# Performance work log

Hardware: AMD Instinct MI355X
Metric: run time of the kernel (lower is better)

## Reference

```python
import jax, jax.numpy as jnp
import numpy as np

N_EMBED = 2048
N_HEAD = 16
HEAD_DIM = N_EMBED // N_HEAD  # 128


def setup_inputs() -> dict:
    key = jax.random.key(0)
    k1, k2, k3 = jax.random.split(key, 3)
    B, S = 2, 2048
    x = jax.random.normal(k1, (B, S, N_EMBED), dtype=jnp.float32)
    # torch Linear weight [out,in]; store transposed for x @ W
    scale_attn = 1.0 / np.sqrt(N_EMBED)
    w_attn = jax.random.normal(k2, (N_EMBED, (N_HEAD + 2) * HEAD_DIM), dtype=jnp.float32) * scale_attn
    w_out = jax.random.normal(k3, (N_EMBED, N_EMBED), dtype=jnp.float32) * scale_attn
    return {"x": x, "w_attn": w_attn, "w_out": w_out}


def reference(x, w_attn, w_out):
    B, S, E = x.shape
    H, D = N_HEAD, HEAD_DIM
    qkv = x @ w_attn                               # [B,S,(H+2)*D]
    q, k, v = jnp.split(qkv, [E, E + D], axis=2)   # [B,S,E], [B,S,D], [B,S,D]
    q = q.reshape(B, S, H, D).transpose(0, 2, 1, 3)  # [B,H,S,D]
    # single shared K/V head (MQA)
    scores = jnp.einsum("bhsd,btd->bhst", q, k) * (D ** -0.5)  # [B,H,S,S]
    p = jax.nn.softmax(scores, axis=-1)
    attn = jnp.einsum("bhst,btd->bhsd", p, v)      # [B,H,S,D]
    attn = attn.transpose(0, 2, 1, 3).reshape(B, S, E)
    return attn @ w_out
```

## Files before the change

### kernel.cpp

```cpp
#include <hip/hip_runtime.h>
#include <hip/hip_bf16.h>

typedef __attribute__((ext_vector_type(8))) short short8;
typedef __attribute__((ext_vector_type(4))) float f32x4;

#define GLOBAL_AS __attribute__((address_space(1)))
#define LDS_AS    __attribute__((address_space(3)))

__device__ __forceinline__ unsigned short f2bf(float f) {
    union { float f; unsigned int u; } v; v.f = f;
    unsigned int r = v.u + 0x7FFFu + ((v.u >> 16) & 1u);
    return (unsigned short)(r >> 16);
}

__device__ __forceinline__ unsigned int pk_bf16(float a, float b) {
    union { __hip_bfloat162 h; unsigned int u; } c;
    c.h = __float22bfloat162_rn(float2{a, b});
    return c.u;
}

__device__ __forceinline__ short8 cvt8v(float4 a, float4 b) {
    union { short8 s; unsigned int u[4]; } c;
    c.u[0] = pk_bf16(a.x, a.y); c.u[1] = pk_bf16(a.z, a.w);
    c.u[2] = pk_bf16(b.x, b.y); c.u[3] = pk_bf16(b.z, b.w);
    return c.s;
}

__device__ __forceinline__ void async_ld16(const unsigned short* g, unsigned short* l) {
    __builtin_amdgcn_global_load_lds((const GLOBAL_AS unsigned int*)g,
                                     (LDS_AS unsigned int*)l, 16, 0, 0);
}

__global__ __launch_bounds__(256) void cvt_bf16(
    const float* __restrict__ src, unsigned short* __restrict__ dst)
{
    const size_t i = ((size_t)blockIdx.x * 256 + threadIdx.x) * 8;
    float4 a = *(const float4*)(src + i);
    float4 b = *(const float4*)(src + i + 4);
    *(short8*)(dst + i) = cvt8v(a, b);
}

__global__ __launch_bounds__(256) void transpose_cvt(
    const float* __restrict__ src, unsigned short* __restrict__ dst, int K, int N)
{
    __shared__ unsigned short t[64][72];
    const int tid = threadIdx.x;
    const int n0 = blockIdx.x * 64, k0 = blockIdx.y * 64;
    #pragma unroll
    for (int it = 0; it < 4; ++it) {
        int r = it * 16 + (tid >> 4);
        int c = (tid & 15) * 4;
        float4 v = *(const float4*)(src + (size_t)(k0 + r) * N + n0 + c);
        t[r][c] = f2bf(v.x); t[r][c + 1] = f2bf(v.y);
        t[r][c + 2] = f2bf(v.z); t[r][c + 3] = f2bf(v.w);
    }
    __syncthreads();
    const int nr = tid >> 2, kg = (tid & 3) * 16;
    short8 o0, o1;
    #pragma unroll
    for (int j = 0; j < 8; ++j) { o0[j] = (short)t[kg + j][nr]; o1[j] = (short)t[kg + 8 + j][nr]; }
    *(short8*)(dst + (size_t)(n0 + nr) * K + k0 + kg) = o0;
    *(short8*)(dst + (size_t)(n0 + nr) * K + k0 + kg + 8) = o1;
}

template<bool OUT_F32>
__global__ __launch_bounds__(256, 3) void gemm_bt(
    const unsigned short* __restrict__ Ab, const unsigned short* __restrict__ Bt,
    void* __restrict__ Cv, int M, int N, int K)
{
    __shared__ __align__(16) unsigned short As[128][64];
    __shared__ __align__(16) unsigned short Bs[128][64];

    const int tid = threadIdx.x, lane = tid & 63, w = tid >> 6;
    const int quad = lane >> 4, l15 = lane & 15;

    const int nwg = gridDim.x * gridDim.y;
    int lin = blockIdx.y * gridDim.x + blockIdx.x;
    lin = (lin & 7) * (nwg >> 3) + (lin >> 3);
    const int m0 = (lin / gridDim.x) * 128, n0 = (lin % gridDim.x) * 128;

    const int rw = (w >> 1) * 64, cw = (w & 1) * 64;

    const f32x4 zero = {0.f, 0.f, 0.f, 0.f};
    f32x4 acc[4][4];
    #pragma unroll
    for (int i = 0; i < 4; ++i)
        #pragma unroll
        for (int j = 0; j < 4; ++j) acc[i][j] = zero;

    const int srow = lane >> 3;
    const int scol = ((lane & 7) ^ srow) * 8;

    const unsigned short* Asf = &As[0][0];
    const unsigned short* Bsf = &Bs[0][0];
    const int rx = (l15 & 7) << 3;

    #pragma unroll
    for (int c = 0; c < 4; ++c)
        async_ld16(Ab + (size_t)(m0 + w * 32 + c * 8 + srow) * K + scol,
                   &As[w * 32 + c * 8][0]);
    #pragma unroll
    for (int c = 0; c < 4; ++c)
        async_ld16(Bt + (size_t)(n0 + w * 32 + c * 8 + srow) * K + scol,
                   &Bs[w * 32 + c * 8][0]);

    for (int k0 = 0; k0 < K; k0 += 64) {
        __syncthreads();

        short8 af[4][2], bf2[4][2];
        #pragma unroll
        for (int i = 0; i < 4; ++i) {
            const int rb = (rw + i * 16 + l15) * 64;
            af[i][0] = *(const short8*)(Asf + ((rb + quad * 8) ^ rx));
            af[i][1] = *(const short8*)(Asf + ((rb + 32 + quad * 8) ^ rx));
        }
        #pragma unroll
        for (int j = 0; j < 4; ++j) {
            const int rb = (cw + j * 16 + l15) * 64;
            bf2[j][0] = *(const short8*)(Bsf + ((rb + quad * 8) ^ rx));
            bf2[j][1] = *(const short8*)(Bsf + ((rb + 32 + quad * 8) ^ rx));
        }
        __syncthreads();

        if (k0 + 64 < K) {
            #pragma unroll
            for (int c = 0; c < 4; ++c)
                async_ld16(Ab + (size_t)(m0 + w * 32 + c * 8 + srow) * K + k0 + 64 + scol,
                           &As[w * 32 + c * 8][0]);
            #pragma unroll
            for (int c = 0; c < 4; ++c)
                async_ld16(Bt + (size_t)(n0 + w * 32 + c * 8 + srow) * K + k0 + 64 + scol,
                           &Bs[w * 32 + c * 8][0]);
        }

        #pragma unroll
        for (int i = 0; i < 4; ++i)
            #pragma unroll
            for (int j = 0; j < 4; ++j) {
                acc[i][j] = __builtin_amdgcn_mfma_f32_16x16x32_bf16(af[i][0], bf2[j][0], acc[i][j], 0, 0, 0);
                acc[i][j] = __builtin_amdgcn_mfma_f32_16x16x32_bf16(af[i][1], bf2[j][1], acc[i][j], 0, 0, 0);
            }
    }

    #pragma unroll
    for (int i = 0; i < 4; ++i) {
        const int row = m0 + rw + i * 16 + quad * 4;
        #pragma unroll
        for (int j = 0; j < 4; ++j) {
            const int col = n0 + cw + j * 16 + l15;
            #pragma unroll
            for (int r = 0; r < 4; ++r) {
                if constexpr (OUT_F32)
                    ((float*)Cv)[(size_t)(row + r) * N + col] = acc[i][j][r];
                else
                    ((unsigned short*)Cv)[(size_t)(row + r) * N + col] = f2bf(acc[i][j][r]);
            }
        }
    }
}

__global__ __launch_bounds__(256) void mqa_flash(
    const unsigned short* __restrict__ qkv,
    unsigned short* __restrict__ attn)
{
    const int S = 2048, QKVW = 2304;
    __shared__ __align__(16) union {
        struct {
            unsigned short Ks[2][32][136];
            unsigned short VT[2][144][44];
        } s;
        unsigned short T[4][32][136];
    } sm;

    const int tid = threadIdx.x, lane = tid & 63, w = tid >> 6;
    const int quad = lane >> 4, l15 = lane & 15;
    const int bid = blockIdx.x;
    const int qb = bid & 15;
    const int h  = (bid >> 4) & 15;
    const int b  = bid >> 8;

    for (int i = tid; i < 2 * 16 * 32; i += 256)
        sm.s.VT[i >> 9][128 + ((i >> 5) & 15)][i & 31] = 0x3F80;

    const unsigned short* base = qkv + (size_t)b * S * QKVW;

    short8 qf[2][4];
    #pragma unroll
    for (int sub = 0; sub < 2; ++sub) {
        const int row = qb * 128 + w * 32 + sub * 16 + l15;
        #pragma unroll
        for (int ds = 0; ds < 4; ++ds)
            qf[sub][ds] = *(const short8*)(base + (size_t)row * QKVW + h * 128 + ds * 32 + quad * 8);
    }

    const f32x4 zero = {0.f, 0.f, 0.f, 0.f};
    f32x4 o[2][9];
    #pragma unroll
    for (int sub = 0; sub < 2; ++sub)
        #pragma unroll
        for (int d = 0; d < 9; ++d) o[sub][d] = zero;

    const int krow = tid & 31, kdg = tid >> 5;
    const int kpr  = ((krow & 1) << 4) | (krow >> 1);
    const int vkp  = tid & 15, vdg = tid >> 4;

    const unsigned short* kp = base + (size_t)krow * QKVW + 2048 + kdg * 16;
    const unsigned short* vp = base + (size_t)(2 * vkp) * QKVW + 2176 + vdg * 8;

    short8 k0v = *(const short8*)kp;
    short8 k1v = *(const short8*)(kp + 8);
    short8 v0v = *(const short8*)vp;
    short8 v1v = *(const short8*)(vp + QKVW);

    for (int kb = 0; kb < S; kb += 32) {
        const int p = (kb >> 5) & 1;

        *(short8*)(&sm.s.Ks[p][kpr][kdg * 16]) = k0v;
        *(short8*)(&sm.s.Ks[p][kpr][kdg * 16 + 8]) = k1v;
        #pragma unroll
        for (int j = 0; j < 8; ++j) {
            unsigned int pkv = (unsigned int)(unsigned short)v0v[j]
                             | ((unsigned int)(unsigned short)v1v[j] << 16);
            *(unsigned int*)(&sm.s.VT[p][vdg * 8 + j][vkp * 2]) = pkv;
        }

        if (kb + 32 < S) {
            kp += 32 * QKVW; vp += 32 * QKVW;
            k0v = *(const short8*)kp;
            k1v = *(const short8*)(kp + 8);
            v0v = *(const short8*)vp;
            v1v = *(const short8*)(vp + QKVW);
        }

        __syncthreads();

        __builtin_amdgcn_s_setprio(1);

        f32x4 sc[2][2];
        sc[0][0] = zero; sc[0][1] = zero; sc[1][0] = zero; sc[1][1] = zero;
        #pragma unroll
        for (int ds = 0; ds < 4; ++ds) {
            short8 kf0 = *(const short8*)(&sm.s.Ks[p][l15][ds * 32 + quad * 8]);
            short8 kf1 = *(const short8*)(&sm.s.Ks[p][16 + l15][ds * 32 + quad * 8]);
            #pragma unroll
            for (int sub = 0; sub < 2; ++sub) {
                sc[sub][0] = __builtin_amdgcn_mfma_f32_16x16x32_bf16(kf0, qf[sub][ds], sc[sub][0], 0, 0, 0);
                sc[sub][1] = __builtin_amdgcn_mfma_f32_16x16x32_bf16(kf1, qf[sub][ds], sc[sub][1], 0, 0, 0);
            }
        }

        const float scale = 0.08838834764831845f;
        short8 pf[2];
        #pragma unroll
        for (int sub = 0; sub < 2; ++sub) {
            union { short8 sv; unsigned int u[4]; } c;
            #pragma unroll
            for (int r = 0; r < 4; ++r) {
                float e0 = __expf(fmaf(sc[sub][0][r], scale, -12.f));
                float e1 = __expf(fmaf(sc[sub][1][r], scale, -12.f));
                c.u[r] = pk_bf16(e0, e1);
            }
            pf[sub] = c.sv;
        }

        #pragma unroll
        for (int dsub = 0; dsub < 9; ++dsub) {
            short8 vf = *(const short8*)(&sm.s.VT[p][dsub * 16 + l15][quad * 8]);
            o[0][dsub] = __builtin_amdgcn_mfma_f32_16x16x32_bf16(vf, pf[0], o[0][dsub], 0, 0, 0);
            o[1][dsub] = __builtin_amdgcn_mfma_f32_16x16x32_bf16(vf, pf[1], o[1][dsub], 0, 0, 0);
        }

        __builtin_amdgcn_s_setprio(0);
    }

    __syncthreads();

    #pragma unroll
    for (int sub = 0; sub < 2; ++sub) {
        const float inv = 1.0f / o[sub][8][0];
        #pragma unroll
        for (int dsub = 0; dsub < 8; ++dsub) {
            unsigned int lo = pk_bf16(o[sub][dsub][0] * inv, o[sub][dsub][1] * inv);
            unsigned int hi = pk_bf16(o[sub][dsub][2] * inv, o[sub][dsub][3] * inv);
            unsigned int* dst = (unsigned int*)&sm.T[w][sub * 16 + l15][dsub * 16 + quad * 4];
            dst[0] = lo; dst[1] = hi;
        }
    }
    __syncthreads();

    const size_t rowbase = (size_t)b * S + qb * 128 + w * 32;
    #pragma unroll
    for (int pass = 0; pass < 8; ++pass) {
        const int row = pass * 4 + quad;
        short8 ov = *(const short8*)(&sm.T[w][row][l15 * 8]);
        *(short8*)(&attn[(rowbase + row) * 2048 + h * 128 + l15 * 8]) = ov;
    }
}

extern "C" void kernel_launch(void* const* d_in, const int* in_sizes, int n_in,
                              void* d_out, int out_size, void* d_ws, size_t ws_size,
                              hipStream_t stream)
{
    const float* x     = (const float*)d_in[0];
    const float* wattn = (const float*)d_in[1];
    const float* wout  = (const float*)d_in[2];
    float* out = (float*)d_out;

    unsigned short* ws = (unsigned short*)d_ws;
    unsigned short* qkv    = ws;
    unsigned short* woutT  = ws;
    unsigned short* wattnT = ws + (size_t)9437184;
    unsigned short* attn   = ws + (size_t)9437184;
    unsigned short* xb     = (unsigned short*)d_out;

    cvt_bf16<<<dim3(4096), 256, 0, stream>>>(x, xb);
    transpose_cvt<<<dim3(2304 / 64, 2048 / 64), 256, 0, stream>>>(wattn, wattnT, 2048, 2304);
    gemm_bt<false><<<dim3(2304 / 128, 4096 / 128), 256, 0, stream>>>(
        xb, wattnT, qkv, 4096, 2304, 2048);
    mqa_flash<<<dim3(2 * 16 * 16), 256, 0, stream>>>(qkv, attn);
    transpose_cvt<<<dim3(2048 / 64, 2048 / 64), 256, 0, stream>>>(wout, woutT, 2048, 2048);
    gemm_bt<true><<<dim3(2048 / 128, 4096 / 128), 256, 0, stream>>>(
        attn, woutT, out, 4096, 2048, 2048);
}
```

Baseline: 277.8 us.

## Add triple-buffered 128x256 async-load GEMM for output projection

Adds a new GEMM kernel for the output projection. It uses a 128x256 tile with 512 threads (8 waves) and three LDS stages filled through async global-to-LDS loads, with an XOR swizzle on LDS addresses. It also remaps workgroups across groups of eight and raises wave priority around the MFMA blocks. The goal is to hide global load latency behind compute and improve tile reuse. The K loop count is hardcoded to K=2048, so the kernel only works for this shape.

```diff
diff --git a/kernel.cpp b/kernel.cpp
--- a/kernel.cpp
+++ b/kernel.cpp
@@ -30,6 +30,9 @@
     __builtin_amdgcn_global_load_lds((const GLOBAL_AS unsigned int*)g,
                                      (LDS_AS unsigned int*)l, 16, 0, 0);
 }
+
+#define WAITV(N) asm volatile("s_waitcnt vmcnt(" #N ")" ::: "memory")
+#define BARSYNC() do { __builtin_amdgcn_s_barrier(); __builtin_amdgcn_sched_barrier(0); } while (0)
 
 __global__ __launch_bounds__(256) void cvt_bf16(
     const float* __restrict__ src, unsigned short* __restrict__ dst)
@@ -155,6 +158,112 @@
                 else
                     ((unsigned short*)Cv)[(size_t)(row + r) * N + col] = f2bf(acc[i][j][r]);
             }
+        }
+    }
+}
+
+__device__ __forceinline__ void stg2(
+    const unsigned short* __restrict__ Ag, const unsigned short* __restrict__ Bg,
+    unsigned short (*Asb)[32], unsigned short (*Bsb)[32],
+    int m0, int n0, int K, int k, int w, int lane)
+{
+    const int r4 = lane >> 2;
+    const int cc = ((lane & 3) ^ (r4 & 3)) * 8;
+    async_ld16(Ag + (size_t)(m0 + w * 16 + r4) * K + k + cc, &Asb[w * 16][0]);
+    #pragma unroll
+    for (int c = 0; c < 2; ++c)
+        async_ld16(Bg + (size_t)(n0 + c * 128 + w * 16 + r4) * K + k + cc,
+                   &Bsb[c * 128 + w * 16][0]);
+}
+
+__device__ __forceinline__ void cmp2(
+    const unsigned short (*Asb)[32], const unsigned short (*Bsb)[32],
+    int wm, int wn, int l15, int quad, f32x4 acc[4][4])
+{
+    const int pc = (quad ^ (l15 & 3)) * 8;
+    short8 af[4], bf[4];
+    #pragma unroll
+    for (int i = 0; i < 4; ++i)
+        af[i] = *(const short8*)&Asb[wm * 64 + i * 16 + l15][pc];
+    #pragma unroll
+    for (int j = 0; j < 4; ++j)
+        bf[j] = *(const short8*)&Bsb[wn * 64 + j * 16 + l15][pc];
+    __builtin_amdgcn_s_setprio(1);
+    #pragma unroll
+    for (int i = 0; i < 4; ++i)
+        #pragma unroll
+        for (int j = 0; j < 4; ++j)
+            acc[i][j] = __builtin_amdgcn_mfma_f32_16x16x32_bf16(af[i], bf[j], acc[i][j], 0, 0, 0);
+    __builtin_amdgcn_s_setprio(0);
+}
+
+__global__ __launch_bounds__(512, 2) void gemm_bn256(
+    const unsigned short* __restrict__ Ab, const unsigned short* __restrict__ Bt,
+    float* __restrict__ Cv, int M, int N, int K)
+{
+    __shared__ __align__(16) unsigned short As0[128][32], As1[128][32], As2[128][32];
+    __shared__ __align__(16) unsigned short Bs0[256][32], Bs1[256][32], Bs2[256][32];
+
+    const int tid = threadIdx.x, lane = tid & 63, w = tid >> 6;
+    const int quad = lane >> 4, l15 = lane & 15;
+    const int wm = w >> 2, wn = w & 3;
+
+    const int nwg = gridDim.x * gridDim.y;
+    int lin = blockIdx.y * gridDim.x + blockIdx.x;
+    lin = (lin & 7) * (nwg >> 3) + (lin >> 3);
+    const int m0 = (lin / gridDim.x) * 128, n0 = (lin % gridDim.x) * 256;
+
+    const f32x4 zero = {0.f, 0.f, 0.f, 0.f};
+    f32x4 acc[4][4];
+    #pragma unroll
+    for (int i = 0; i < 4; ++i)
+        #pragma unroll
+        for (int j = 0; j < 4; ++j) acc[i][j] = zero;
+
+    stg2(Ab, Bt, As0, Bs0, m0, n0, K, 0,  w, lane);
+    stg2(Ab, Bt, As1, Bs1, m0, n0, K, 32, w, lane);
+
+    int t = 0;
+    #pragma unroll 1
+    for (int it = 0; it < 20; ++it) {
+        WAITV(3); BARSYNC();
+        stg2(Ab, Bt, As2, Bs2, m0, n0, K, (t + 2) * 32, w, lane);
+        cmp2(As0, Bs0, wm, wn, l15, quad, acc);
+
+        WAITV(3); BARSYNC();
+        stg2(Ab, Bt, As0, Bs0, m0, n0, K, (t + 3) * 32, w, lane);
+        cmp2(As1, Bs1, wm, wn, l15, quad, acc);
+
+        WAITV(3); BARSYNC();
+        stg2(Ab, Bt, As1, Bs1, m0, n0, K, (t + 4) * 32, w, lane);
+        cmp2(As2, Bs2, wm, wn, l15, quad, acc);
+
+        t += 3;
+    }
+
+    WAITV(3); BARSYNC();
+    stg2(Ab, Bt, As2, Bs2, m0, n0, K, 62 * 32, w, lane);
+    cmp2(As0, Bs0, wm, wn, l15, quad, acc);
+
+    WAITV(3); BARSYNC();
+    stg2(Ab, Bt, As0, Bs0, m0, n0, K, 63 * 32, w, lane);
+    cmp2(As1, Bs1, wm, wn, l15, quad, acc);
+
+    WAITV(3); BARSYNC();
+    cmp2(As2, Bs2, wm, wn, l15, quad, acc);
+
+    WAITV(0); BARSYNC();
+    cmp2(As0, Bs0, wm, wn, l15, quad, acc);
+
+    #pragma unroll
+    for (int i = 0; i < 4; ++i) {
+        const int row = m0 + wm * 64 + i * 16 + quad * 4;
+        #pragma unroll
+        for (int j = 0; j < 4; ++j) {
+            const int col = n0 + wn * 64 + j * 16 + l15;
+            #pragma unroll
+            for (int r = 0; r < 4; ++r)
+                Cv[(size_t)(row + r) * N + col] = acc[i][j][r];
         }
     }
 }
@@ -319,6 +428,6 @@
         xb, wattnT, qkv, 4096, 2304, 2048);
     mqa_flash<<<dim3(2 * 16 * 16), 256, 0, stream>>>(qkv, attn);
     transpose_cvt<<<dim3(2048 / 64, 2048 / 64), 256, 0, stream>>>(wout, woutT, 2048, 2048);
-    gemm_bt<true><<<dim3(2048 / 128, 4096 / 128), 256, 0, stream>>>(
+    gemm_bn256<<<dim3(2048 / 256, 4096 / 128), 512, 0, stream>>>(
         attn, woutT, out, 4096, 2048, 2048);
 }
```

Result: no change. 274.6 us (-1.1%).
